# Performance work log

Measured on AMD Instinct MI355X. Metric: run time of the kernel, lower is better.

The kernel has to match this reference:

```python
import jax, jax.numpy as jnp
import numpy as np

NUM_QUANT_BITS = 8


def setup_inputs() -> dict:
    key = jax.random.key(0)
    x = jax.random.normal(key, (64, 56, 56, 256), dtype=jnp.float32)
    return {"x": x}


def reference(x):
    # Global range (min_val/max_val default to None in the original layer)
    min_val = jnp.min(x)
    max_val = jnp.max(x)
    quantized_range = jnp.asarray(2 ** NUM_QUANT_BITS - 1, dtype=x.dtype)  # 255
    scale = quantized_range / (max_val - min_val)
    xc = jnp.clip(x, min_val, max_val)
    # round-to-nearest-even matches tf.round semantics
    out = jnp.round((xc - min_val) * scale) / scale + min_val
    return out
```

## Files before the change

### kernel.cpp

```cpp
#include <hip/hip_runtime.h>
#include <stdint.h>
#include <math.h>

__device__ __forceinline__ uint32_t enc_f32(float f) {
    uint32_t b = __float_as_uint(f);
    return (b & 0x80000000u) ? ~b : (b | 0x80000000u);
}
__device__ __forceinline__ float dec_f32(uint32_t u) {
    uint32_t b = (u & 0x80000000u) ? (u ^ 0x80000000u) : ~u;
    return __uint_as_float(b);
}

__global__ void init_ws_kernel(uint32_t* ws) {
    ws[0] = 0xFFFFFFFFu;
    ws[1] = 0x00000000u;
}

__global__ __launch_bounds__(256) void minmax_kernel(
    const float4* __restrict__ x4, long n4,
    const float* __restrict__ x, long n,
    uint32_t* __restrict__ ws)
{
    float mn = INFINITY, mx = -INFINITY;
    const long stride = (long)gridDim.x * blockDim.x;
    for (long i = (long)blockIdx.x * blockDim.x + threadIdx.x; i < n4; i += stride) {
        float4 v = x4[i];
        mn = fminf(mn, fminf(fminf(v.x, v.y), fminf(v.z, v.w)));
        mx = fmaxf(mx, fmaxf(fmaxf(v.x, v.y), fmaxf(v.z, v.w)));
    }
    for (long i = n4 * 4 + (long)blockIdx.x * blockDim.x + threadIdx.x; i < n; i += stride) {
        float v = x[i];
        mn = fminf(mn, v);
        mx = fmaxf(mx, v);
    }
    #pragma unroll
    for (int off = 32; off > 0; off >>= 1) {
        mn = fminf(mn, __shfl_down(mn, off, 64));
        mx = fmaxf(mx, __shfl_down(mx, off, 64));
    }
    __shared__ float smn[4], smx[4];
    const int wave = threadIdx.x >> 6;
    const int lane = threadIdx.x & 63;
    if (lane == 0) { smn[wave] = mn; smx[wave] = mx; }
    __syncthreads();
    if (threadIdx.x == 0) {
        const int nw = blockDim.x >> 6;
        mn = smn[0]; mx = smx[0];
        for (int w = 1; w < nw; ++w) {
            mn = fminf(mn, smn[w]);
            mx = fmaxf(mx, smx[w]);
        }
        atomicMin(&ws[0], enc_f32(mn));
        atomicMax(&ws[1], enc_f32(mx));
    }
}

__global__ __launch_bounds__(256) void quant_kernel(
    const float4* __restrict__ x4, long n4,
    const float* __restrict__ x, long n,
    float4* __restrict__ o4, float* __restrict__ o,
    const uint32_t* __restrict__ ws)
{
    const float mn = dec_f32(ws[0]);
    const float mx = dec_f32(ws[1]);
    const float scale = 255.0f / (mx - mn);
    const float inv_scale = 1.0f / scale;
    const long stride = (long)gridDim.x * blockDim.x;
    for (long i = (long)blockIdx.x * blockDim.x + threadIdx.x; i < n4; i += stride) {
        float4 v = x4[i];
        float4 r;
        r.x = rintf((v.x - mn) * scale) * inv_scale + mn;
        r.y = rintf((v.y - mn) * scale) * inv_scale + mn;
        r.z = rintf((v.z - mn) * scale) * inv_scale + mn;
        r.w = rintf((v.w - mn) * scale) * inv_scale + mn;
        o4[i] = r;
    }
    for (long i = n4 * 4 + (long)blockIdx.x * blockDim.x + threadIdx.x; i < n; i += stride) {
        o[i] = rintf((x[i] - mn) * scale) * inv_scale + mn;
    }
}

extern "C" void kernel_launch(void* const* d_in, const int* in_sizes, int n_in,
                              void* d_out, int out_size, void* d_ws, size_t ws_size,
                              hipStream_t stream) {
    const float* x = (const float*)d_in[0];
    float* out = (float*)d_out;
    const long n = (long)in_sizes[0];
    const long n4 = n / 4;
    uint32_t* ws = (uint32_t*)d_ws;

    init_ws_kernel<<<1, 1, 0, stream>>>(ws);

    const int block = 256;
    const int grid = 4096;
    minmax_kernel<<<grid, block, 0, stream>>>((const float4*)x, n4, x, n, ws);
    quant_kernel<<<grid, block, 0, stream>>>((const float4*)x, n4, x, n,
                                             (float4*)out, out, ws);
}
```

Before: 434.1 us.

## Unroll streaming loops 4x, use nontemporal stores, 32-bit indexing, halve grid

Both the min/max and quantize kernels now process four float4 vectors per thread per iteration, with independent accumulators so more loads are in flight. Output writes use nontemporal stores so the output stream does not pollute the cache. Indices switch to 32-bit, the grid size is halved, and scalar tails move to separate tiny kernels. The risks are more registers per thread, fewer blocks in flight to hide memory latency, and 32-bit indices that would overflow on very large inputs.

```diff
diff --git a/kernel.cpp b/kernel.cpp
--- a/kernel.cpp
+++ b/kernel.cpp
@@ -1,6 +1,8 @@
 #include <hip/hip_runtime.h>
 #include <stdint.h>
 #include <math.h>
+
+typedef float vf4 __attribute__((ext_vector_type(4)));
 
 __device__ __forceinline__ uint32_t enc_f32(float f) {
     uint32_t b = __float_as_uint(f);
@@ -16,23 +18,39 @@
     ws[1] = 0x00000000u;
 }
 
+__device__ __forceinline__ void mm4(vf4 v, float& mn, float& mx) {
+    mn = fminf(mn, fminf(fminf(v.x, v.y), fminf(v.z, v.w)));
+    mx = fmaxf(mx, fmaxf(fmaxf(v.x, v.y), fmaxf(v.z, v.w)));
+}
+
 __global__ __launch_bounds__(256) void minmax_kernel(
-    const float4* __restrict__ x4, long n4,
-    const float* __restrict__ x, long n,
+    const vf4* __restrict__ x4, unsigned n4,
     uint32_t* __restrict__ ws)
 {
-    float mn = INFINITY, mx = -INFINITY;
-    const long stride = (long)gridDim.x * blockDim.x;
-    for (long i = (long)blockIdx.x * blockDim.x + threadIdx.x; i < n4; i += stride) {
-        float4 v = x4[i];
-        mn = fminf(mn, fminf(fminf(v.x, v.y), fminf(v.z, v.w)));
-        mx = fmaxf(mx, fmaxf(fmaxf(v.x, v.y), fmaxf(v.z, v.w)));
+    float mn0 = INFINITY, mn1 = INFINITY, mn2 = INFINITY, mn3 = INFINITY;
+    float mx0 = -INFINITY, mx1 = -INFINITY, mx2 = -INFINITY, mx3 = -INFINITY;
+
+    const unsigned bs = blockDim.x;
+    const unsigned stride = gridDim.x * bs * 4u;
+    unsigned base = blockIdx.x * bs * 4u + threadIdx.x;
+
+    for (; base + 3u * bs < n4; base += stride) {
+        vf4 v0 = x4[base];
+        vf4 v1 = x4[base + bs];
+        vf4 v2 = x4[base + 2u * bs];
+        vf4 v3 = x4[base + 3u * bs];
+        mm4(v0, mn0, mx0);
+        mm4(v1, mn1, mx1);
+        mm4(v2, mn2, mx2);
+        mm4(v3, mn3, mx3);
     }
-    for (long i = n4 * 4 + (long)blockIdx.x * blockDim.x + threadIdx.x; i < n; i += stride) {
-        float v = x[i];
-        mn = fminf(mn, v);
-        mx = fmaxf(mx, v);
+    for (; base < n4; base += bs) {
+        mm4(x4[base], mn0, mx0);
     }
+
+    float mn = fminf(fminf(mn0, mn1), fminf(mn2, mn3));
+    float mx = fmaxf(fmaxf(mx0, mx1), fmaxf(mx2, mx3));
+
     #pragma unroll
     for (int off = 32; off > 0; off >>= 1) {
         mn = fminf(mn, __shfl_down(mn, off, 64));
@@ -44,39 +62,71 @@
     if (lane == 0) { smn[wave] = mn; smx[wave] = mx; }
     __syncthreads();
     if (threadIdx.x == 0) {
-        const int nw = blockDim.x >> 6;
-        mn = smn[0]; mx = smx[0];
-        for (int w = 1; w < nw; ++w) {
-            mn = fminf(mn, smn[w]);
-            mx = fmaxf(mx, smx[w]);
-        }
+        mn = fminf(fminf(smn[0], smn[1]), fminf(smn[2], smn[3]));
+        mx = fmaxf(fmaxf(smx[0], smx[1]), fmaxf(smx[2], smx[3]));
         atomicMin(&ws[0], enc_f32(mn));
         atomicMax(&ws[1], enc_f32(mx));
     }
 }
 
+__device__ __forceinline__ vf4 q4(vf4 v, float mn, float scale, float inv_scale) {
+    vf4 r;
+    r.x = rintf((v.x - mn) * scale) * inv_scale + mn;
+    r.y = rintf((v.y - mn) * scale) * inv_scale + mn;
+    r.z = rintf((v.z - mn) * scale) * inv_scale + mn;
+    r.w = rintf((v.w - mn) * scale) * inv_scale + mn;
+    return r;
+}
+
 __global__ __launch_bounds__(256) void quant_kernel(
-    const float4* __restrict__ x4, long n4,
-    const float* __restrict__ x, long n,
-    float4* __restrict__ o4, float* __restrict__ o,
+    const vf4* __restrict__ x4, unsigned n4,
+    vf4* __restrict__ o4,
     const uint32_t* __restrict__ ws)
 {
     const float mn = dec_f32(ws[0]);
     const float mx = dec_f32(ws[1]);
     const float scale = 255.0f / (mx - mn);
     const float inv_scale = 1.0f / scale;
-    const long stride = (long)gridDim.x * blockDim.x;
-    for (long i = (long)blockIdx.x * blockDim.x + threadIdx.x; i < n4; i += stride) {
-        float4 v = x4[i];
-        float4 r;
-        r.x = rintf((v.x - mn) * scale) * inv_scale + mn;
-        r.y = rintf((v.y - mn) * scale) * inv_scale + mn;
-        r.z = rintf((v.z - mn) * scale) * inv_scale + mn;
-        r.w = rintf((v.w - mn) * scale) * inv_scale + mn;
-        o4[i] = r;
+
+    const unsigned bs = blockDim.x;
+    const unsigned stride = gridDim.x * bs * 4u;
+    unsigned base = blockIdx.x * bs * 4u + threadIdx.x;
+
+    for (; base + 3u * bs < n4; base += stride) {
+        vf4 v0 = x4[base];
+        vf4 v1 = x4[base + bs];
+        vf4 v2 = x4[base + 2u * bs];
+        vf4 v3 = x4[base + 3u * bs];
+        __builtin_nontemporal_store(q4(v0, mn, scale, inv_scale), &o4[base]);
+        __builtin_nontemporal_store(q4(v1, mn, scale, inv_scale), &o4[base + bs]);
+        __builtin_nontemporal_store(q4(v2, mn, scale, inv_scale), &o4[base + 2u * bs]);
+        __builtin_nontemporal_store(q4(v3, mn, scale, inv_scale), &o4[base + 3u * bs]);
     }
-    for (long i = n4 * 4 + (long)blockIdx.x * blockDim.x + threadIdx.x; i < n; i += stride) {
-        o[i] = rintf((x[i] - mn) * scale) * inv_scale + mn;
+    for (; base < n4; base += bs) {
+        __builtin_nontemporal_store(q4(x4[base], mn, scale, inv_scale), &o4[base]);
+    }
+}
+
+__global__ void quant_tail_kernel(const float* __restrict__ x, long start, long n,
+                                  float* __restrict__ o,
+                                  const uint32_t* __restrict__ ws)
+{
+    const float mn = dec_f32(ws[0]);
+    const float mx = dec_f32(ws[1]);
+    const float scale = 255.0f / (mx - mn);
+    const float inv_scale = 1.0f / scale;
+    long i = start + threadIdx.x;
+    if (i < n) o[i] = rintf((x[i] - mn) * scale) * inv_scale + mn;
+}
+
+__global__ void minmax_tail_kernel(const float* __restrict__ x, long start, long n,
+                                   uint32_t* __restrict__ ws)
+{
+    long i = start + threadIdx.x;
+    if (i < n) {
+        float v = x[i];
+        atomicMin(&ws[0], enc_f32(v));
+        atomicMax(&ws[1], enc_f32(v));
     }
 }
 
@@ -86,14 +136,17 @@
     const float* x = (const float*)d_in[0];
     float* out = (float*)d_out;
     const long n = (long)in_sizes[0];
-    const long n4 = n / 4;
+    const unsigned n4 = (unsigned)(n / 4);
     uint32_t* ws = (uint32_t*)d_ws;
 
     init_ws_kernel<<<1, 1, 0, stream>>>(ws);
 
     const int block = 256;
-    const int grid = 4096;
-    minmax_kernel<<<grid, block, 0, stream>>>((const float4*)x, n4, x, n, ws);
-    quant_kernel<<<grid, block, 0, stream>>>((const float4*)x, n4, x, n,
-                                             (float4*)out, out, ws);
+    const int grid = 2048;
+
+    minmax_kernel<<<grid, block, 0, stream>>>((const vf4*)x, n4, ws);
+    if (n % 4) minmax_tail_kernel<<<1, 256, 0, stream>>>(x, (long)n4 * 4, n, ws);
+
+    quant_kernel<<<grid, block, 0, stream>>>((const vf4*)x, n4, (vf4*)out, ws);
+    if (n % 4) quant_tail_kernel<<<1, 256, 0, stream>>>(x, (long)n4 * 4, n, out, ws);
 }
```

After: 376.0 us. 1.15x faster.
